# Kernel optimization log

Measured on AMD Instinct MI355X. Metric: run time of the kernel, lower is better.

Reference implementation:

```python
import jax, jax.numpy as jnp
import numpy as np

N = 10000
H_INPUTS = 128
H = 512
RW_LEN = 16
BATCH = 512


def setup_inputs() -> dict:
    key = jax.random.key(0)
    ks = jax.random.split(key, 5)
    x = jax.random.normal(ks[0], (BATCH, RW_LEN, N + 1), dtype=jnp.float32)
    # xavier-ish scaled params
    W_down = jax.random.normal(ks[1], (N, H_INPUTS), dtype=jnp.float32) * (1.0 / np.sqrt(N))
    W_cell = jax.random.normal(ks[2], (H_INPUTS + 1 + H, 4 * H), dtype=jnp.float32) * (1.0 / np.sqrt(H_INPUTS + 1 + H))
    b_cell = jnp.zeros((4 * H,), dtype=jnp.float32)
    W_out = jax.random.normal(ks[3], (H, 1), dtype=jnp.float32) * (1.0 / np.sqrt(H))
    b_out = jnp.zeros((1,), dtype=jnp.float32)
    return {"x": x, "W_down": W_down, "W_cell": W_cell, "b_cell": b_cell,
            "W_out": W_out, "b_out": b_out}


def _forward(x, W_down, W_cell, b_cell, W_out, b_out):
    B = x.shape[0]
    x_rw = x[:, :, :N]                       # [B, T, N]
    x_weights = x[:, :, -1:]                 # [B, T, 1]
    xa = jnp.einsum('btn,nh->bth', x_rw, W_down)  # down-projection [B, T, H_in]
    xc = jnp.concatenate([xa, x_weights], axis=2)  # [B, T, H_in+1]
    xc_t = jnp.swapaxes(xc, 0, 1)            # [T, B, H_in+1] for scan

    h0 = jnp.zeros((B, H), dtype=x.dtype)
    c0 = jnp.zeros((B, H), dtype=x.dtype)

    def step(carry, xt):
        h, c = carry
        gates = jnp.concatenate([xt, h], axis=1) @ W_cell + b_cell  # [B, 4H]
        i_g, c_g, f_g, o_g = jnp.split(gates, 4, axis=1)
        # custom forget-gate bias of +1
        c_new = c * jax.nn.sigmoid(f_g + 1.0) + jax.nn.sigmoid(i_g) * jnp.tanh(c_g)
        h_new = jax.nn.sigmoid(o_g) * jnp.tanh(c_new)
        return (h_new, c_new), None

    (h, _), _ = jax.lax.scan(step, (h0, c0), xc_t)
    pred = h @ W_out + b_out                 # [B, 1]
    return pred


def reference(x, W_down, W_cell, b_cell, W_out, b_out):
    return _forward(x, W_down, W_cell, b_cell, W_out, b_out)
```

## Files before the change

### kernel.cpp

```cpp
#include <hip/hip_runtime.h>
#include <cmath>

#define TID ((int)threadIdx.x)

typedef __bf16 bf16_t;
typedef bf16_t bf16x8 __attribute__((ext_vector_type(8)));
typedef float floatx4 __attribute__((ext_vector_type(4)));

#define MFMA(a, b, c) __builtin_amdgcn_mfma_f32_16x16x32_bf16(a, b, c, 0, 0, 0)

constexpr int N_IN = 10000;
constexpr int XP   = 10001;
constexpr int KPD  = 10240;
constexpr int HH   = 512;
constexpr int TT   = 16;
constexpr int NB   = 512;
constexpr int MROW = 8192;
constexpr int KSPLIT = 16;
constexpr int KCHUNK = 640;
constexpr int KT_A = 10;

__device__ __forceinline__ float sigm(float x) { return 1.0f / (1.0f + expf(-x)); }

__device__ __forceinline__ void gload16(const void* g, void* lds) {
  __builtin_amdgcn_global_load_lds(
      (const __attribute__((address_space(1))) unsigned int*)g,
      (__attribute__((address_space(3))) unsigned int*)lds, 16, 0, 0);
}

__global__ __launch_bounds__(256)
void kPrepWd(const float* __restrict__ Wd, bf16_t* __restrict__ Whi, bf16_t* __restrict__ Wlo) {
  __shared__ float Ts[64][133];
  const int k0 = blockIdx.x * 64;
  #pragma unroll
  for (int i = 0; i < 32; ++i) {
    int f = TID + 256 * i;
    int kk = f >> 7, c = f & 127;
    int k = k0 + kk;
    Ts[kk][c] = (k < N_IN) ? Wd[(size_t)k * 128 + c] : 0.0f;
  }
  __syncthreads();
  const int lane = TID & 63, w = TID >> 6;
  for (int pass = 0; pass < 32; ++pass) {
    int c = pass * 4 + w;
    float v = Ts[lane][c];
    bf16_t hi = (bf16_t)v;
    bf16_t lo = (bf16_t)(v - (float)hi);
    Whi[(size_t)c * KPD + k0 + lane] = hi;
    Wlo[(size_t)c * KPD + k0 + lane] = lo;
  }
}

__global__ __launch_bounds__(256)
void kPrepWc(const float* __restrict__ Wc, bf16_t* __restrict__ Wxh, bf16_t* __restrict__ Wxl,
             float* __restrict__ wN, bf16_t* __restrict__ Whh, bf16_t* __restrict__ Whl) {
  __shared__ float Ts[64][133];
  const int k0 = blockIdx.x * 64;
  const int c0 = blockIdx.y * 128;
  #pragma unroll
  for (int i = 0; i < 32; ++i) {
    int f = TID + 256 * i;
    int kk = f >> 7, cc = f & 127;
    int k = k0 + kk;
    Ts[kk][cc] = (k < 641) ? Wc[(size_t)k * 2048 + c0 + cc] : 0.0f;
  }
  __syncthreads();
  const int lane = TID & 63, w = TID >> 6;
  const int k = k0 + lane;
  for (int pass = 0; pass < 32; ++pass) {
    int cc = pass * 4 + w;
    int c = c0 + cc;
    float v = Ts[lane][cc];
    bf16_t hi = (bf16_t)v;
    bf16_t lo = (bf16_t)(v - (float)hi);
    if (k < 128) {
      Wxh[(size_t)c * 128 + k] = hi;
      Wxl[(size_t)c * 128 + k] = lo;
    } else if (k == 128) {
      wN[c] = v;
    } else if (k < 641) {
      Whh[(size_t)c * 512 + (k - 129)] = hi;
      Whl[(size_t)c * 512 + (k - 129)] = lo;
    }
  }
}

__global__ __launch_bounds__(256)
void kPrepXw(const float* __restrict__ x, float* __restrict__ xw) {
  int r = blockIdx.x * 256 + TID;
  xw[r] = x[(size_t)r * XP + N_IN];
}

__global__ __launch_bounds__(256, 2)
void kA_mfma(const float* __restrict__ x, const bf16_t* __restrict__ Whi,
             const bf16_t* __restrict__ Wlo, float* __restrict__ parts) {
  __shared__ __align__(16) bf16_t Bt[2][2048 * 8];
  const int lane = TID & 63, w = TID >> 6;
  const int row0 = blockIdx.x * 128 + w * 32;
  const int kbase = blockIdx.y * KCHUNK;
  floatx4 acc[2][8] = {};

  auto STAGE = [&](int buf, int kt) {
    const int k0 = kbase + kt * 64;
    #pragma unroll
    for (int i = 0; i < 8; ++i) {
      int L = i * 256 + TID;
      int arr = L >> 10, col = (L >> 3) & 127, g = L & 7;
      int gs = g ^ (col & 7);
      const bf16_t* src = (arr ? Wlo : Whi) + (size_t)col * KPD + k0 + gs * 8;
      gload16(src, &Bt[buf][(size_t)L * 8]);
    }
  };
  auto LOADX = [&](float4 (&xb)[2][2][2], int kt) {
    const int k0 = kbase + kt * 64;
    #pragma unroll
    for (int rf = 0; rf < 2; ++rf) {
      const float* xp = x + (size_t)(row0 + rf * 16 + (lane & 15)) * XP;
      #pragma unroll
      for (int h = 0; h < 2; ++h) {
        int kk0 = k0 + h * 32 + (lane >> 4) * 8;
        if (kk0 < N_IN) {
          xb[rf][h][0] = *(const float4*)(xp + kk0);
          xb[rf][h][1] = *(const float4*)(xp + kk0 + 4);
        } else {
          xb[rf][h][0] = make_float4(0.f, 0.f, 0.f, 0.f);
          xb[rf][h][1] = make_float4(0.f, 0.f, 0.f, 0.f);
        }
      }
    }
  };
  auto COMPUTE = [&](int buf, const float4 (&xb)[2][2][2]) {
    #pragma unroll
    for (int h = 0; h < 2; ++h) {
      const int p = h * 4 + (lane >> 4);
      bf16x8 ahi[2], alo[2];
      #pragma unroll
      for (int rf = 0; rf < 2; ++rf) {
        float vv[8] = {xb[rf][h][0].x, xb[rf][h][0].y, xb[rf][h][0].z, xb[rf][h][0].w,
                       xb[rf][h][1].x, xb[rf][h][1].y, xb[rf][h][1].z, xb[rf][h][1].w};
        #pragma unroll
        for (int e = 0; e < 8; ++e) {
          bf16_t hi = (bf16_t)vv[e];
          ahi[rf][e] = hi;
          alo[rf][e] = (bf16_t)(vv[e] - (float)hi);
        }
      }
      #pragma unroll
      for (int cf = 0; cf < 8; ++cf) {
        const int col = cf * 16 + (lane & 15);
        const int g = p ^ (col & 7);
        bf16x8 bhi = *(const bf16x8*)&Bt[buf][(col * 8 + g) * 8];
        bf16x8 blo = *(const bf16x8*)&Bt[buf][(1024 + col * 8 + g) * 8];
        #pragma unroll
        for (int rf = 0; rf < 2; ++rf) {
          acc[rf][cf] = MFMA(ahi[rf], bhi, acc[rf][cf]);
          acc[rf][cf] = MFMA(ahi[rf], blo, acc[rf][cf]);
          acc[rf][cf] = MFMA(alo[rf], bhi, acc[rf][cf]);
        }
      }
    }
  };

  float4 xbA[2][2][2], xbB[2][2][2];
  STAGE(0, 0);
  LOADX(xbA, 0);
  __syncthreads();
  #pragma unroll
  for (int kt = 0; kt < KT_A; kt += 2) {
    if (kt + 1 < KT_A) { STAGE(1, kt + 1); LOADX(xbB, kt + 1); }
    COMPUTE(0, xbA);
    __syncthreads();
    if (kt + 2 < KT_A) { STAGE(0, kt + 2); LOADX(xbA, kt + 2); }
    COMPUTE(1, xbB);
    __syncthreads();
  }

  float* dst = parts + (size_t)blockIdx.y * MROW * 128;
  #pragma unroll
  for (int rf = 0; rf < 2; ++rf)
    #pragma unroll
    for (int cf = 0; cf < 8; ++cf)
      #pragma unroll
      for (int r = 0; r < 4; ++r) {
        int row = row0 + rf * 16 + (lane >> 4) * 4 + r;
        int col = cf * 16 + (lane & 15);
        dst[(size_t)row * 128 + col] = acc[rf][cf][r];
      }
}

__global__ __launch_bounds__(256)
void kRed(const float* __restrict__ parts, float* __restrict__ xa) {
  size_t i4 = ((size_t)blockIdx.x * 256 + TID) * 4;
  float4 v = make_float4(0.f, 0.f, 0.f, 0.f);
  #pragma unroll
  for (int s = 0; s < KSPLIT; ++s) {
    float4 p = *(const float4*)&parts[(size_t)s * MROW * 128 + i4];
    v.x += p.x; v.y += p.y; v.z += p.z; v.w += p.w;
  }
  *(float4*)&xa[i4] = v;
}

__global__ __launch_bounds__(512, 2)
void kGx(const float* __restrict__ xa, const float* __restrict__ xw,
         const bf16_t* __restrict__ Wxh, const bf16_t* __restrict__ Wxl,
         const float* __restrict__ wN, const float* __restrict__ bc,
         float* __restrict__ gx) {
  __shared__ __align__(16) bf16_t Bt[4096 * 8];
  const int lane = TID & 63, w = TID >> 6;
  const int wr = w & 3, wc = w >> 2;
  const int rowbase = blockIdx.x * 128 + wr * 32;
  const int JB = blockIdx.y * 32;
  floatx4 acc[2][4] = {};

  #pragma unroll
  for (int i = 0; i < 8; ++i) {
    int L = i * 512 + TID;
    int arr = L >> 11, ce = (L >> 4) & 127, g = L & 15;
    int gs = g ^ (ce & 15);
    int c_src = (ce & 3) * 512 + JB + (ce >> 2);
    const bf16_t* src = (arr ? Wxl : Wxh) + (size_t)c_src * 128 + gs * 8;
    gload16(src, &Bt[(size_t)L * 8]);
  }
  float4 xb[2][2][2][2];
  #pragma unroll
  for (int kt = 0; kt < 2; ++kt)
    #pragma unroll
    for (int rf = 0; rf < 2; ++rf) {
      const float* ap = xa + (size_t)(rowbase + rf * 16 + (lane & 15)) * 128;
      #pragma unroll
      for (int h = 0; h < 2; ++h) {
        int kk0 = kt * 64 + h * 32 + (lane >> 4) * 8;
        xb[kt][rf][h][0] = *(const float4*)(ap + kk0);
        xb[kt][rf][h][1] = *(const float4*)(ap + kk0 + 4);
      }
    }
  __syncthreads();
  #pragma unroll
  for (int kt = 0; kt < 2; ++kt) {
    #pragma unroll
    for (int h = 0; h < 2; ++h) {
      const int p = kt * 8 + h * 4 + (lane >> 4);
      bf16x8 ahi[2], alo[2];
      #pragma unroll
      for (int rf = 0; rf < 2; ++rf) {
        float vv[8] = {xb[kt][rf][h][0].x, xb[kt][rf][h][0].y, xb[kt][rf][h][0].z, xb[kt][rf][h][0].w,
                       xb[kt][rf][h][1].x, xb[kt][rf][h][1].y, xb[kt][rf][h][1].z, xb[kt][rf][h][1].w};
        #pragma unroll
        for (int e = 0; e < 8; ++e) {
          bf16_t hi = (bf16_t)vv[e];
          ahi[rf][e] = hi;
          alo[rf][e] = (bf16_t)(vv[e] - (float)hi);
        }
      }
      #pragma unroll
      for (int cf = 0; cf < 4; ++cf) {
        const int ce = wc * 64 + cf * 16 + (lane & 15);
        const int g = p ^ (ce & 15);
        bf16x8 bhi = *(const bf16x8*)&Bt[(ce * 16 + g) * 8];
        bf16x8 blo = *(const bf16x8*)&Bt[(2048 + ce * 16 + g) * 8];
        #pragma unroll
        for (int rf = 0; rf < 2; ++rf) {
          acc[rf][cf] = MFMA(ahi[rf], bhi, acc[rf][cf]);
          acc[rf][cf] = MFMA(ahi[rf], blo, acc[rf][cf]);
          acc[rf][cf] = MFMA(alo[rf], bhi, acc[rf][cf]);
        }
      }
    }
  }
  #pragma unroll
  for (int rf = 0; rf < 2; ++rf)
    #pragma unroll
    for (int cf = 0; cf < 4; ++cf) {
      const int ce = wc * 64 + cf * 16 + (lane & 15);
      const int n = blockIdx.y * 128 + ce;
      const int c_src = (ce & 3) * 512 + JB + (ce >> 2);
      const float bias = bc[c_src];
      const float wn = wN[c_src];
      #pragma unroll
      for (int r = 0; r < 4; ++r) {
        int row = rowbase + rf * 16 + (lane >> 4) * 4 + r;
        gx[(size_t)row * 2048 + n] = acc[rf][cf][r] + bias + xw[row] * wn;
      }
    }
}

__global__ __launch_bounds__(128, 2)
void kStepH(const bf16_t* __restrict__ hhi_in, const bf16_t* __restrict__ hlo_in,
            const bf16_t* __restrict__ Whh, const bf16_t* __restrict__ Whl,
            const float* __restrict__ gx, const float* __restrict__ c_in,
            bf16_t* __restrict__ hhi_out, bf16_t* __restrict__ hlo_out,
            float* __restrict__ c_out, int t, int has_h) {
  __shared__ __align__(16) bf16_t Bt[2][1024 * 8];
  const int lane = TID & 63, w = TID >> 6;
  const int j0 = blockIdx.x * 16;
  const int brow0 = blockIdx.y * 64 + w * 32;
  floatx4 acc[2][4] = {};

  auto STAGE = [&](int buf, int kt) {
    const int k0 = kt * 64;
    #pragma unroll
    for (int i = 0; i < 8; ++i) {
      int L = i * 128 + TID;
      int arr = L >> 9, ce = (L >> 3) & 63, g = L & 7;
      int gs = g ^ (ce & 7);
      int c_src = (ce >> 4) * 512 + j0 + (ce & 15);
      const bf16_t* src = (arr ? Whl : Whh) + (size_t)c_src * 512 + k0 + gs * 8;
      gload16(src, &Bt[buf][(size_t)L * 8]);
    }
  };
  auto LOADA = [&](bf16x8 (&ar)[2][2][2], int kt) {
    #pragma unroll
    for (int rf = 0; rf < 2; ++rf) {
      const int b = brow0 + rf * 16 + (lane & 15);
      #pragma unroll
      for (int h = 0; h < 2; ++h) {
        const int kk0 = kt * 64 + h * 32 + (lane >> 4) * 8;
        ar[rf][h][0] = *(const bf16x8*)&hhi_in[(size_t)b * HH + kk0];
        ar[rf][h][1] = *(const bf16x8*)&hlo_in[(size_t)b * HH + kk0];
      }
    }
  };
  auto COMPUTE = [&](int buf, const bf16x8 (&ar)[2][2][2]) {
    #pragma unroll
    for (int h = 0; h < 2; ++h) {
      const int p = h * 4 + (lane >> 4);
      #pragma unroll
      for (int cf = 0; cf < 4; ++cf) {
        const int ce = cf * 16 + (lane & 15);
        const int g = p ^ (ce & 7);
        bf16x8 bhi = *(const bf16x8*)&Bt[buf][(ce * 8 + g) * 8];
        bf16x8 blo = *(const bf16x8*)&Bt[buf][(512 + ce * 8 + g) * 8];
        #pragma unroll
        for (int rf = 0; rf < 2; ++rf) {
          acc[rf][cf] = MFMA(ar[rf][h][0], bhi, acc[rf][cf]);
          acc[rf][cf] = MFMA(ar[rf][h][0], blo, acc[rf][cf]);
          acc[rf][cf] = MFMA(ar[rf][h][1], bhi, acc[rf][cf]);
        }
      }
    }
  };

  if (has_h) {
    bf16x8 aA[2][2][2], aB[2][2][2];
    STAGE(0, 0);
    LOADA(aA, 0);
    __syncthreads();
    #pragma unroll
    for (int kt = 0; kt < 8; kt += 2) {
      if (kt + 1 < 8) { STAGE(1, kt + 1); LOADA(aB, kt + 1); }
      COMPUTE(0, aA);
      __syncthreads();
      if (kt + 2 < 8) { STAGE(0, kt + 2); LOADA(aA, kt + 2); }
      COMPUTE(1, aB);
      __syncthreads();
    }
  }

  const int jl = lane & 15;
  const int j = j0 + jl;
  #pragma unroll
  for (int rf = 0; rf < 2; ++rf)
    #pragma unroll
    for (int r = 0; r < 4; ++r) {
      int b = brow0 + rf * 16 + (lane >> 4) * 4 + r;
      float4 gv = *(const float4*)&gx[((size_t)b * TT + t) * 2048 + (size_t)j * 4];
      float gi = acc[rf][0][r] + gv.x;
      float gc = acc[rf][1][r] + gv.y;
      float gf = acc[rf][2][r] + gv.z;
      float go = acc[rf][3][r] + gv.w;
      float cp = has_h ? c_in[(size_t)b * HH + j] : 0.0f;
      float cn = cp * sigm(gf + 1.0f) + sigm(gi) * tanhf(gc);
      float hn = sigm(go) * tanhf(cn);
      c_out[(size_t)b * HH + j] = cn;
      bf16_t hh = (bf16_t)hn;
      hhi_out[(size_t)b * HH + j] = hh;
      hlo_out[(size_t)b * HH + j] = (bf16_t)(hn - (float)hh);
    }
}

__global__ __launch_bounds__(64)
void kC_out(const bf16_t* __restrict__ hh, const bf16_t* __restrict__ hl,
            const float* __restrict__ Wo, const float* __restrict__ bo,
            float* __restrict__ out) {
  const int b = blockIdx.x;
  float s = 0.0f;
  for (int j = TID; j < HH; j += 64)
    s += ((float)hh[(size_t)b * HH + j] + (float)hl[(size_t)b * HH + j]) * Wo[j];
  #pragma unroll
  for (int off = 32; off > 0; off >>= 1) s += __shfl_down(s, off);
  if (TID == 0) out[b] = s + bo[0];
}

extern "C" void kernel_launch(void* const* d_in, const int* in_sizes, int n_in,
                              void* d_out, int out_size, void* d_ws, size_t ws_size,
                              hipStream_t stream) {
  const float* x  = (const float*)d_in[0];
  const float* Wd = (const float*)d_in[1];
  const float* Wc = (const float*)d_in[2];
  const float* bc = (const float*)d_in[3];
  const float* Wo = (const float*)d_in[4];
  const float* bo = (const float*)d_in[5];
  float* out = (float*)d_out;

  char* wsb = (char*)d_ws;
  size_t off = 0;
  auto alloc = [&](size_t bytes) -> void* {
    void* p = wsb + off;
    off = (off + bytes + 255) & ~(size_t)255;
    return p;
  };
  bf16_t* WdThi = (bf16_t*)alloc((size_t)128 * KPD * 2);
  bf16_t* WdTlo = (bf16_t*)alloc((size_t)128 * KPD * 2);
  bf16_t* WxThi = (bf16_t*)alloc((size_t)2048 * 128 * 2);
  bf16_t* WxTlo = (bf16_t*)alloc((size_t)2048 * 128 * 2);
  bf16_t* WhThi = (bf16_t*)alloc((size_t)2048 * 512 * 2);
  bf16_t* WhTlo = (bf16_t*)alloc((size_t)2048 * 512 * 2);
  float*  wN    = (float*)alloc(2048 * 4);
  float*  xw    = (float*)alloc(MROW * 4);
  float*  xa    = (float*)alloc((size_t)MROW * 128 * 4);
  float*  parts = (float*)alloc((size_t)KSPLIT * MROW * 128 * 4);
  float*  gx    = parts;
  bf16_t* hhi[2] = {(bf16_t*)alloc((size_t)NB * HH * 2), (bf16_t*)alloc((size_t)NB * HH * 2)};
  bf16_t* hlo[2] = {(bf16_t*)alloc((size_t)NB * HH * 2), (bf16_t*)alloc((size_t)NB * HH * 2)};
  float*  cb[2]  = {(float*)alloc((size_t)NB * HH * 4), (float*)alloc((size_t)NB * HH * 4)};

  kPrepWd<<<160, 256, 0, stream>>>(Wd, WdThi, WdTlo);
  kPrepWc<<<dim3(11, 16), 256, 0, stream>>>(Wc, WxThi, WxTlo, wN, WhThi, WhTlo);
  kPrepXw<<<32, 256, 0, stream>>>(x, xw);
  kA_mfma<<<dim3(64, KSPLIT), 256, 0, stream>>>(x, WdThi, WdTlo, parts);
  kRed<<<1024, 256, 0, stream>>>(parts, xa);
  kGx<<<dim3(64, 16), 512, 0, stream>>>(xa, xw, WxThi, WxTlo, wN, bc, gx);
  for (int t = 0; t < TT; ++t) {
    kStepH<<<dim3(32, 8), 128, 0, stream>>>(hhi[t & 1], hlo[t & 1], WhThi, WhTlo,
        gx, cb[t & 1], hhi[(t + 1) & 1], hlo[(t + 1) & 1], cb[(t + 1) & 1],
        t, (t == 0) ? 0 : 1);
  }
  kC_out<<<512, 64, 0, stream>>>(hhi[0], hlo[0], Wo, bo, out);
}
```

Measured before the change: 467.3 us.

## Fuse LSTM timesteps into persistent kernel with grid barrier and resident weights

Replaces the 16 per-step kStepH launches with one persistent kernel of 128 blocks. Each block loads its slice of the recurrent weights into shared memory once and keeps it there, and the blocks synchronise between steps through an atomic grid barrier. The gx layout becomes time-major so each step reads contiguous rows. The down-projection kernel also moves to 32-wide K tiles with a simpler unswizzled LDS layout. This removes per-step launch overhead and the repeated weight restaging, at the cost of depending on all 128 blocks being co-resident and of possible LDS bank conflicts in kA.

```diff
diff --git a/kernel.cpp b/kernel.cpp
--- a/kernel.cpp
+++ b/kernel.cpp
@@ -18,7 +18,8 @@
 constexpr int MROW = 8192;
 constexpr int KSPLIT = 16;
 constexpr int KCHUNK = 640;
-constexpr int KT_A = 10;
+constexpr int KT_A = 20;
+constexpr int NBLK_STEPS = 128;
 
 __device__ __forceinline__ float sigm(float x) { return 1.0f / (1.0f + expf(-x)); }
 
@@ -94,80 +95,72 @@
 __global__ __launch_bounds__(256, 2)
 void kA_mfma(const float* __restrict__ x, const bf16_t* __restrict__ Whi,
              const bf16_t* __restrict__ Wlo, float* __restrict__ parts) {
-  __shared__ __align__(16) bf16_t Bt[2][2048 * 8];
+  __shared__ __align__(16) bf16_t Bt[2 * 1024 * 8];
   const int lane = TID & 63, w = TID >> 6;
   const int row0 = blockIdx.x * 128 + w * 32;
   const int kbase = blockIdx.y * KCHUNK;
   floatx4 acc[2][8] = {};
 
   auto STAGE = [&](int buf, int kt) {
-    const int k0 = kbase + kt * 64;
-    #pragma unroll
-    for (int i = 0; i < 8; ++i) {
+    const int k0 = kbase + kt * 32;
+    #pragma unroll
+    for (int i = 0; i < 4; ++i) {
       int L = i * 256 + TID;
-      int arr = L >> 10, col = (L >> 3) & 127, g = L & 7;
-      int gs = g ^ (col & 7);
-      const bf16_t* src = (arr ? Wlo : Whi) + (size_t)col * KPD + k0 + gs * 8;
-      gload16(src, &Bt[buf][(size_t)L * 8]);
+      int arr = L >> 9, g = (L >> 7) & 3, col = L & 127;
+      const bf16_t* src = (arr ? Wlo : Whi) + (size_t)col * KPD + k0 + g * 8;
+      gload16(src, &Bt[((size_t)buf * 1024 + L) * 8]);
     }
   };
-  auto LOADX = [&](float4 (&xb)[2][2][2], int kt) {
-    const int k0 = kbase + kt * 64;
+  auto LOADX = [&](float4 (&xb)[2][2], int kt) {
+    const int kk0 = kbase + kt * 32 + (lane >> 4) * 8;
     #pragma unroll
     for (int rf = 0; rf < 2; ++rf) {
       const float* xp = x + (size_t)(row0 + rf * 16 + (lane & 15)) * XP;
-      #pragma unroll
-      for (int h = 0; h < 2; ++h) {
-        int kk0 = k0 + h * 32 + (lane >> 4) * 8;
-        if (kk0 < N_IN) {
-          xb[rf][h][0] = *(const float4*)(xp + kk0);
-          xb[rf][h][1] = *(const float4*)(xp + kk0 + 4);
-        } else {
-          xb[rf][h][0] = make_float4(0.f, 0.f, 0.f, 0.f);
-          xb[rf][h][1] = make_float4(0.f, 0.f, 0.f, 0.f);
-        }
+      if (kk0 < N_IN) {
+        xb[rf][0] = *(const float4*)(xp + kk0);
+        xb[rf][1] = *(const float4*)(xp + kk0 + 4);
+      } else {
+        xb[rf][0] = make_float4(0.f, 0.f, 0.f, 0.f);
+        xb[rf][1] = make_float4(0.f, 0.f, 0.f, 0.f);
       }
     }
   };
-  auto COMPUTE = [&](int buf, const float4 (&xb)[2][2][2]) {
-    #pragma unroll
-    for (int h = 0; h < 2; ++h) {
-      const int p = h * 4 + (lane >> 4);
-      bf16x8 ahi[2], alo[2];
+  auto COMPUTE = [&](int buf, const float4 (&xb)[2][2]) {
+    const int p = lane >> 4;
+    bf16x8 ahi[2], alo[2];
+    #pragma unroll
+    for (int rf = 0; rf < 2; ++rf) {
+      float vv[8] = {xb[rf][0].x, xb[rf][0].y, xb[rf][0].z, xb[rf][0].w,
+                     xb[rf][1].x, xb[rf][1].y, xb[rf][1].z, xb[rf][1].w};
+      #pragma unroll
+      for (int e = 0; e < 8; ++e) {
+        bf16_t hi = (bf16_t)vv[e];
+        ahi[rf][e] = hi;
+        alo[rf][e] = (bf16_t)(vv[e] - (float)hi);
+      }
+    }
+    #pragma unroll
+    for (int cf = 0; cf < 8; ++cf) {
+      const int col = cf * 16 + (lane & 15);
+      bf16x8 bhi = *(const bf16x8*)&Bt[((size_t)buf * 1024 + p * 128 + col) * 8];
+      bf16x8 blo = *(const bf16x8*)&Bt[((size_t)buf * 1024 + 512 + p * 128 + col) * 8];
       #pragma unroll
       for (int rf = 0; rf < 2; ++rf) {
-        float vv[8] = {xb[rf][h][0].x, xb[rf][h][0].y, xb[rf][h][0].z, xb[rf][h][0].w,
-                       xb[rf][h][1].x, xb[rf][h][1].y, xb[rf][h][1].z, xb[rf][h][1].w};
-        #pragma unroll
-        for (int e = 0; e < 8; ++e) {
-          bf16_t hi = (bf16_t)vv[e];
-          ahi[rf][e] = hi;
-          alo[rf][e] = (bf16_t)(vv[e] - (float)hi);
-        }
-      }
-      #pragma unroll
-      for (int cf = 0; cf < 8; ++cf) {
-        const int col = cf * 16 + (lane & 15);
-        const int g = p ^ (col & 7);
-        bf16x8 bhi = *(const bf16x8*)&Bt[buf][(col * 8 + g) * 8];
-        bf16x8 blo = *(const bf16x8*)&Bt[buf][(1024 + col * 8 + g) * 8];
-        #pragma unroll
-        for (int rf = 0; rf < 2; ++rf) {
-          acc[rf][cf] = MFMA(ahi[rf], bhi, acc[rf][cf]);
-          acc[rf][cf] = MFMA(ahi[rf], blo, acc[rf][cf]);
-          acc[rf][cf] = MFMA(alo[rf], bhi, acc[rf][cf]);
-        }
+        acc[rf][cf] = MFMA(ahi[rf], bhi, acc[rf][cf]);
+        acc[rf][cf] = MFMA(ahi[rf], blo, acc[rf][cf]);
+        acc[rf][cf] = MFMA(alo[rf], bhi, acc[rf][cf]);
       }
     }
   };
 
-  float4 xbA[2][2][2], xbB[2][2][2];
+  float4 xbA[2][2], xbB[2][2];
   STAGE(0, 0);
   LOADX(xbA, 0);
   __syncthreads();
   #pragma unroll
   for (int kt = 0; kt < KT_A; kt += 2) {
-    if (kt + 1 < KT_A) { STAGE(1, kt + 1); LOADX(xbB, kt + 1); }
+    STAGE(1, kt + 1);
+    LOADX(xbB, kt + 1);
     COMPUTE(0, xbA);
     __syncthreads();
     if (kt + 2 < KT_A) { STAGE(0, kt + 2); LOADX(xbA, kt + 2); }
@@ -279,103 +272,120 @@
       #pragma unroll
       for (int r = 0; r < 4; ++r) {
         int row = rowbase + rf * 16 + (lane >> 4) * 4 + r;
-        gx[(size_t)row * 2048 + n] = acc[rf][cf][r] + bias + xw[row] * wn;
-      }
-    }
-}
-
-__global__ __launch_bounds__(128, 2)
-void kStepH(const bf16_t* __restrict__ hhi_in, const bf16_t* __restrict__ hlo_in,
-            const bf16_t* __restrict__ Whh, const bf16_t* __restrict__ Whl,
-            const float* __restrict__ gx, const float* __restrict__ c_in,
-            bf16_t* __restrict__ hhi_out, bf16_t* __restrict__ hlo_out,
-            float* __restrict__ c_out, int t, int has_h) {
-  __shared__ __align__(16) bf16_t Bt[2][1024 * 8];
+        int b = row >> 4, tt = row & 15;
+        gx[((size_t)tt * NB + b) * 2048 + n] = acc[rf][cf][r] + bias + xw[row] * wn;
+      }
+    }
+}
+
+__global__ __launch_bounds__(256, 1)
+void kSteps(const bf16_t* __restrict__ Whh, const bf16_t* __restrict__ Whl,
+            const float* __restrict__ gx,
+            bf16_t* __restrict__ h0hi, bf16_t* __restrict__ h0lo,
+            bf16_t* __restrict__ h1hi, bf16_t* __restrict__ h1lo,
+            float* __restrict__ c0, float* __restrict__ c1,
+            unsigned* __restrict__ bar) {
+  __shared__ __align__(16) bf16_t Bt[8192 * 8];
   const int lane = TID & 63, w = TID >> 6;
   const int j0 = blockIdx.x * 16;
-  const int brow0 = blockIdx.y * 64 + w * 32;
-  floatx4 acc[2][4] = {};
-
-  auto STAGE = [&](int buf, int kt) {
-    const int k0 = kt * 64;
-    #pragma unroll
-    for (int i = 0; i < 8; ++i) {
-      int L = i * 128 + TID;
-      int arr = L >> 9, ce = (L >> 3) & 63, g = L & 7;
-      int gs = g ^ (ce & 7);
-      int c_src = (ce >> 4) * 512 + j0 + (ce & 15);
-      const bf16_t* src = (arr ? Whl : Whh) + (size_t)c_src * 512 + k0 + gs * 8;
-      gload16(src, &Bt[buf][(size_t)L * 8]);
-    }
-  };
-  auto LOADA = [&](bf16x8 (&ar)[2][2][2], int kt) {
-    #pragma unroll
-    for (int rf = 0; rf < 2; ++rf) {
-      const int b = brow0 + rf * 16 + (lane & 15);
-      #pragma unroll
-      for (int h = 0; h < 2; ++h) {
-        const int kk0 = kt * 64 + h * 32 + (lane >> 4) * 8;
-        ar[rf][h][0] = *(const bf16x8*)&hhi_in[(size_t)b * HH + kk0];
-        ar[rf][h][1] = *(const bf16x8*)&hlo_in[(size_t)b * HH + kk0];
-      }
-    }
-  };
-  auto COMPUTE = [&](int buf, const bf16x8 (&ar)[2][2][2]) {
-    #pragma unroll
-    for (int h = 0; h < 2; ++h) {
-      const int p = h * 4 + (lane >> 4);
-      #pragma unroll
-      for (int cf = 0; cf < 4; ++cf) {
-        const int ce = cf * 16 + (lane & 15);
-        const int g = p ^ (ce & 7);
-        bf16x8 bhi = *(const bf16x8*)&Bt[buf][(ce * 8 + g) * 8];
-        bf16x8 blo = *(const bf16x8*)&Bt[buf][(512 + ce * 8 + g) * 8];
+  const int brow0 = blockIdx.y * 128 + w * 32;
+
+  for (int i = 0; i < 32; ++i) {
+    int L = i * 256 + TID;
+    int kt = L >> 10, arr = (L >> 9) & 1, ce = (L >> 3) & 63, g = L & 7;
+    int gs = g ^ (ce & 7);
+    int c_src = (ce >> 4) * 512 + j0 + (ce & 15);
+    const bf16_t* src = (arr ? Whl : Whh) + (size_t)c_src * 512 + kt * 64 + gs * 8;
+    gload16(src, &Bt[(size_t)L * 8]);
+  }
+  __syncthreads();
+
+  bf16_t* hhi[2] = {h0hi, h1hi};
+  bf16_t* hlo[2] = {h0lo, h1lo};
+  float*  cb[2]  = {c0, c1};
+
+  #pragma unroll 1
+  for (int t = 0; t < TT; ++t) {
+    floatx4 acc[2][4] = {};
+    if (t > 0) {
+      __syncthreads();
+      if (TID == 0) {
+        __threadfence();
+        __hip_atomic_fetch_add(bar, 1u, __ATOMIC_ACQ_REL, __HIP_MEMORY_SCOPE_AGENT);
+        const unsigned target = (unsigned)t * NBLK_STEPS;
+        while (__hip_atomic_load(bar, __ATOMIC_ACQUIRE, __HIP_MEMORY_SCOPE_AGENT) < target) {
+          __builtin_amdgcn_s_sleep(8);
+        }
+        __threadfence();
+      }
+      __syncthreads();
+      const bf16_t* hi_in = hhi[t & 1];
+      const bf16_t* lo_in = hlo[t & 1];
+      auto LOADA = [&](bf16x8 (&ar)[2][2][2], int kt) {
         #pragma unroll
         for (int rf = 0; rf < 2; ++rf) {
-          acc[rf][cf] = MFMA(ar[rf][h][0], bhi, acc[rf][cf]);
-          acc[rf][cf] = MFMA(ar[rf][h][0], blo, acc[rf][cf]);
-          acc[rf][cf] = MFMA(ar[rf][h][1], bhi, acc[rf][cf]);
+          const int b = brow0 + rf * 16 + (lane & 15);
+          #pragma unroll
+          for (int h = 0; h < 2; ++h) {
+            const int kk0 = kt * 64 + h * 32 + (lane >> 4) * 8;
+            ar[rf][h][0] = *(const bf16x8*)&hi_in[(size_t)b * HH + kk0];
+            ar[rf][h][1] = *(const bf16x8*)&lo_in[(size_t)b * HH + kk0];
+          }
         }
-      }
-    }
-  };
-
-  if (has_h) {
-    bf16x8 aA[2][2][2], aB[2][2][2];
-    STAGE(0, 0);
-    LOADA(aA, 0);
-    __syncthreads();
-    #pragma unroll
-    for (int kt = 0; kt < 8; kt += 2) {
-      if (kt + 1 < 8) { STAGE(1, kt + 1); LOADA(aB, kt + 1); }
-      COMPUTE(0, aA);
-      __syncthreads();
-      if (kt + 2 < 8) { STAGE(0, kt + 2); LOADA(aA, kt + 2); }
-      COMPUTE(1, aB);
-      __syncthreads();
-    }
-  }
-
-  const int jl = lane & 15;
-  const int j = j0 + jl;
-  #pragma unroll
-  for (int rf = 0; rf < 2; ++rf)
-    #pragma unroll
-    for (int r = 0; r < 4; ++r) {
-      int b = brow0 + rf * 16 + (lane >> 4) * 4 + r;
-      float4 gv = *(const float4*)&gx[((size_t)b * TT + t) * 2048 + (size_t)j * 4];
-      float gi = acc[rf][0][r] + gv.x;
-      float gc = acc[rf][1][r] + gv.y;
-      float gf = acc[rf][2][r] + gv.z;
-      float go = acc[rf][3][r] + gv.w;
-      float cp = has_h ? c_in[(size_t)b * HH + j] : 0.0f;
-      float cn = cp * sigm(gf + 1.0f) + sigm(gi) * tanhf(gc);
-      float hn = sigm(go) * tanhf(cn);
-      c_out[(size_t)b * HH + j] = cn;
-      bf16_t hh = (bf16_t)hn;
-      hhi_out[(size_t)b * HH + j] = hh;
-      hlo_out[(size_t)b * HH + j] = (bf16_t)(hn - (float)hh);
-    }
+      };
+      auto COMPUTE = [&](int kt, const bf16x8 (&ar)[2][2][2]) {
+        #pragma unroll
+        for (int h = 0; h < 2; ++h) {
+          const int p = h * 4 + (lane >> 4);
+          #pragma unroll
+          for (int cf = 0; cf < 4; ++cf) {
+            const int ce = cf * 16 + (lane & 15);
+            const int g = p ^ (ce & 7);
+            bf16x8 bhi = *(const bf16x8*)&Bt[((size_t)kt * 1024 + ce * 8 + g) * 8];
+            bf16x8 blo = *(const bf16x8*)&Bt[((size_t)kt * 1024 + 512 + ce * 8 + g) * 8];
+            #pragma unroll
+            for (int rf = 0; rf < 2; ++rf) {
+              acc[rf][cf] = MFMA(ar[rf][h][0], bhi, acc[rf][cf]);
+              acc[rf][cf] = MFMA(ar[rf][h][0], blo, acc[rf][cf]);
+              acc[rf][cf] = MFMA(ar[rf][h][1], bhi, acc[rf][cf]);
+            }
+          }
+        }
+      };
+      bf16x8 aA[2][2][2], aB[2][2][2];
+      LOADA(aA, 0);
+      #pragma unroll
+      for (int kt = 0; kt < 8; kt += 2) {
+        LOADA(aB, kt + 1);
+        COMPUTE(kt, aA);
+        if (kt + 2 < 8) LOADA(aA, kt + 2);
+        COMPUTE(kt + 1, aB);
+      }
+    }
+    const int j = j0 + (lane & 15);
+    const float* cin = cb[t & 1];
+    float* cout = cb[(t + 1) & 1];
+    bf16_t* hho = hhi[(t + 1) & 1];
+    bf16_t* hlo_o = hlo[(t + 1) & 1];
+    #pragma unroll
+    for (int rf = 0; rf < 2; ++rf)
+      #pragma unroll
+      for (int r = 0; r < 4; ++r) {
+        int b = brow0 + rf * 16 + (lane >> 4) * 4 + r;
+        float4 gv = *(const float4*)&gx[((size_t)t * NB + b) * 2048 + (size_t)j * 4];
+        float gi = acc[rf][0][r] + gv.x;
+        float gc = acc[rf][1][r] + gv.y;
+        float gf = acc[rf][2][r] + gv.z;
+        float go = acc[rf][3][r] + gv.w;
+        float cp = (t > 0) ? cin[(size_t)b * HH + j] : 0.0f;
+        float cn = cp * sigm(gf + 1.0f) + sigm(gi) * tanhf(gc);
+        float hn = sigm(go) * tanhf(cn);
+        cout[(size_t)b * HH + j] = cn;
+        bf16_t hh = (bf16_t)hn;
+        hho[(size_t)b * HH + j] = hh;
+        hlo_o[(size_t)b * HH + j] = (bf16_t)(hn - (float)hh);
+      }
+  }
 }
 
 __global__ __launch_bounds__(64)
@@ -420,20 +430,22 @@
   float*  xa    = (float*)alloc((size_t)MROW * 128 * 4);
   float*  parts = (float*)alloc((size_t)KSPLIT * MROW * 128 * 4);
   float*  gx    = parts;
-  bf16_t* hhi[2] = {(bf16_t*)alloc((size_t)NB * HH * 2), (bf16_t*)alloc((size_t)NB * HH * 2)};
-  bf16_t* hlo[2] = {(bf16_t*)alloc((size_t)NB * HH * 2), (bf16_t*)alloc((size_t)NB * HH * 2)};
-  float*  cb[2]  = {(float*)alloc((size_t)NB * HH * 4), (float*)alloc((size_t)NB * HH * 4)};
-
+  bf16_t* h0hi = (bf16_t*)alloc((size_t)NB * HH * 2);
+  bf16_t* h0lo = (bf16_t*)alloc((size_t)NB * HH * 2);
+  bf16_t* h1hi = (bf16_t*)alloc((size_t)NB * HH * 2);
+  bf16_t* h1lo = (bf16_t*)alloc((size_t)NB * HH * 2);
+  float*  c0   = (float*)alloc((size_t)NB * HH * 4);
+  float*  c1   = (float*)alloc((size_t)NB * HH * 4);
+  unsigned* bar = (unsigned*)alloc(256);
+
+  hipMemsetAsync(bar, 0, 256, stream);
   kPrepWd<<<160, 256, 0, stream>>>(Wd, WdThi, WdTlo);
   kPrepWc<<<dim3(11, 16), 256, 0, stream>>>(Wc, WxThi, WxTlo, wN, WhThi, WhTlo);
   kPrepXw<<<32, 256, 0, stream>>>(x, xw);
   kA_mfma<<<dim3(64, KSPLIT), 256, 0, stream>>>(x, WdThi, WdTlo, parts);
   kRed<<<1024, 256, 0, stream>>>(parts, xa);
   kGx<<<dim3(64, 16), 512, 0, stream>>>(xa, xw, WxThi, WxTlo, wN, bc, gx);
-  for (int t = 0; t < TT; ++t) {
-    kStepH<<<dim3(32, 8), 128, 0, stream>>>(hhi[t & 1], hlo[t & 1], WhThi, WhTlo,
-        gx, cb[t & 1], hhi[(t + 1) & 1], hlo[(t + 1) & 1], cb[(t + 1) & 1],
-        t, (t == 0) ? 0 : 1);
-  }
-  kC_out<<<512, 64, 0, stream>>>(hhi[0], hlo[0], Wo, bo, out);
-}
+  kSteps<<<dim3(32, 4), 256, 0, stream>>>(WhThi, WhTlo, gx,
+      h0hi, h0lo, h1hi, h1lo, c0, c1, bar);
+  kC_out<<<512, 64, 0, stream>>>(h0hi, h0lo, Wo, bo, out);
+}
```

Result: slower. 653.4 us (+39.8%).

## Halve kA k-tile with linear LDS layout and make gx time-major

Applied to the files above, without the earlier changes.

The down-projection kernel now stages 32-wide k-tiles instead of 64, which halves the LDS footprint. It drops the XOR swizzle in favour of a plain group-major layout and runs twice as many pipeline iterations. The gate-input buffer gx is rewritten in [t][b][n] order so each recurrent step reads a contiguous slab. The goal is higher occupancy in kA and better locality in the step kernels, at the cost of more barriers and possible LDS bank conflicts without the swizzle.

```diff
diff --git a/kernel.cpp b/kernel.cpp
--- a/kernel.cpp
+++ b/kernel.cpp
@@ -18,7 +18,7 @@
 constexpr int MROW = 8192;
 constexpr int KSPLIT = 16;
 constexpr int KCHUNK = 640;
-constexpr int KT_A = 10;
+constexpr int KT_A = 20;
 
 __device__ __forceinline__ float sigm(float x) { return 1.0f / (1.0f + expf(-x)); }
 
@@ -94,80 +94,72 @@
 __global__ __launch_bounds__(256, 2)
 void kA_mfma(const float* __restrict__ x, const bf16_t* __restrict__ Whi,
              const bf16_t* __restrict__ Wlo, float* __restrict__ parts) {
-  __shared__ __align__(16) bf16_t Bt[2][2048 * 8];
+  __shared__ __align__(16) bf16_t Bt[2 * 1024 * 8];
   const int lane = TID & 63, w = TID >> 6;
   const int row0 = blockIdx.x * 128 + w * 32;
   const int kbase = blockIdx.y * KCHUNK;
   floatx4 acc[2][8] = {};
 
   auto STAGE = [&](int buf, int kt) {
-    const int k0 = kbase + kt * 64;
-    #pragma unroll
-    for (int i = 0; i < 8; ++i) {
+    const int k0 = kbase + kt * 32;
+    #pragma unroll
+    for (int i = 0; i < 4; ++i) {
       int L = i * 256 + TID;
-      int arr = L >> 10, col = (L >> 3) & 127, g = L & 7;
-      int gs = g ^ (col & 7);
-      const bf16_t* src = (arr ? Wlo : Whi) + (size_t)col * KPD + k0 + gs * 8;
-      gload16(src, &Bt[buf][(size_t)L * 8]);
-    }
-  };
-  auto LOADX = [&](float4 (&xb)[2][2][2], int kt) {
-    const int k0 = kbase + kt * 64;
+      int arr = L >> 9, g = (L >> 7) & 3, col = L & 127;
+      const bf16_t* src = (arr ? Wlo : Whi) + (size_t)col * KPD + k0 + g * 8;
+      gload16(src, &Bt[((size_t)buf * 1024 + L) * 8]);
+    }
+  };
+  auto LOADX = [&](float4 (&xb)[2][2], int kt) {
+    const int kk0 = kbase + kt * 32 + (lane >> 4) * 8;
     #pragma unroll
     for (int rf = 0; rf < 2; ++rf) {
       const float* xp = x + (size_t)(row0 + rf * 16 + (lane & 15)) * XP;
-      #pragma unroll
-      for (int h = 0; h < 2; ++h) {
-        int kk0 = k0 + h * 32 + (lane >> 4) * 8;
-        if (kk0 < N_IN) {
-          xb[rf][h][0] = *(const float4*)(xp + kk0);
-          xb[rf][h][1] = *(const float4*)(xp + kk0 + 4);
-        } else {
-          xb[rf][h][0] = make_float4(0.f, 0.f, 0.f, 0.f);
-          xb[rf][h][1] = make_float4(0.f, 0.f, 0.f, 0.f);
-        }
-      }
-    }
-  };
-  auto COMPUTE = [&](int buf, const float4 (&xb)[2][2][2]) {
-    #pragma unroll
-    for (int h = 0; h < 2; ++h) {
-      const int p = h * 4 + (lane >> 4);
-      bf16x8 ahi[2], alo[2];
+      if (kk0 < N_IN) {
+        xb[rf][0] = *(const float4*)(xp + kk0);
+        xb[rf][1] = *(const float4*)(xp + kk0 + 4);
+      } else {
+        xb[rf][0] = make_float4(0.f, 0.f, 0.f, 0.f);
+        xb[rf][1] = make_float4(0.f, 0.f, 0.f, 0.f);
+      }
+    }
+  };
+  auto COMPUTE = [&](int buf, const float4 (&xb)[2][2]) {
+    const int p = lane >> 4;
+    bf16x8 ahi[2], alo[2];
+    #pragma unroll
+    for (int rf = 0; rf < 2; ++rf) {
+      float vv[8] = {xb[rf][0].x, xb[rf][0].y, xb[rf][0].z, xb[rf][0].w,
+                     xb[rf][1].x, xb[rf][1].y, xb[rf][1].z, xb[rf][1].w};
+      #pragma unroll
+      for (int e = 0; e < 8; ++e) {
+        bf16_t hi = (bf16_t)vv[e];
+        ahi[rf][e] = hi;
+        alo[rf][e] = (bf16_t)(vv[e] - (float)hi);
+      }
+    }
+    #pragma unroll
+    for (int cf = 0; cf < 8; ++cf) {
+      const int col = cf * 16 + (lane & 15);
+      bf16x8 bhi = *(const bf16x8*)&Bt[((size_t)buf * 1024 + p * 128 + col) * 8];
+      bf16x8 blo = *(const bf16x8*)&Bt[((size_t)buf * 1024 + 512 + p * 128 + col) * 8];
       #pragma unroll
       for (int rf = 0; rf < 2; ++rf) {
-        float vv[8] = {xb[rf][h][0].x, xb[rf][h][0].y, xb[rf][h][0].z, xb[rf][h][0].w,
-                       xb[rf][h][1].x, xb[rf][h][1].y, xb[rf][h][1].z, xb[rf][h][1].w};
-        #pragma unroll
-        for (int e = 0; e < 8; ++e) {
-          bf16_t hi = (bf16_t)vv[e];
-          ahi[rf][e] = hi;
-          alo[rf][e] = (bf16_t)(vv[e] - (float)hi);
-        }
-      }
-      #pragma unroll
-      for (int cf = 0; cf < 8; ++cf) {
-        const int col = cf * 16 + (lane & 15);
-        const int g = p ^ (col & 7);
-        bf16x8 bhi = *(const bf16x8*)&Bt[buf][(col * 8 + g) * 8];
-        bf16x8 blo = *(const bf16x8*)&Bt[buf][(1024 + col * 8 + g) * 8];
-        #pragma unroll
-        for (int rf = 0; rf < 2; ++rf) {
-          acc[rf][cf] = MFMA(ahi[rf], bhi, acc[rf][cf]);
-          acc[rf][cf] = MFMA(ahi[rf], blo, acc[rf][cf]);
-          acc[rf][cf] = MFMA(alo[rf], bhi, acc[rf][cf]);
-        }
-      }
-    }
-  };
-
-  float4 xbA[2][2][2], xbB[2][2][2];
+        acc[rf][cf] = MFMA(ahi[rf], bhi, acc[rf][cf]);
+        acc[rf][cf] = MFMA(ahi[rf], blo, acc[rf][cf]);
+        acc[rf][cf] = MFMA(alo[rf], bhi, acc[rf][cf]);
+      }
+    }
+  };
+
+  float4 xbA[2][2], xbB[2][2];
   STAGE(0, 0);
   LOADX(xbA, 0);
   __syncthreads();
   #pragma unroll
   for (int kt = 0; kt < KT_A; kt += 2) {
-    if (kt + 1 < KT_A) { STAGE(1, kt + 1); LOADX(xbB, kt + 1); }
+    STAGE(1, kt + 1);
+    LOADX(xbB, kt + 1);
     COMPUTE(0, xbA);
     __syncthreads();
     if (kt + 2 < KT_A) { STAGE(0, kt + 2); LOADX(xbA, kt + 2); }
@@ -279,7 +271,8 @@
       #pragma unroll
       for (int r = 0; r < 4; ++r) {
         int row = rowbase + rf * 16 + (lane >> 4) * 4 + r;
-        gx[(size_t)row * 2048 + n] = acc[rf][cf][r] + bias + xw[row] * wn;
+        int b = row >> 4, tt = row & 15;
+        gx[((size_t)tt * NB + b) * 2048 + n] = acc[rf][cf][r] + bias + xw[row] * wn;
       }
     }
 }
@@ -356,14 +349,13 @@
     }
   }
 
-  const int jl = lane & 15;
-  const int j = j0 + jl;
+  const int j = j0 + (lane & 15);
   #pragma unroll
   for (int rf = 0; rf < 2; ++rf)
     #pragma unroll
     for (int r = 0; r < 4; ++r) {
       int b = brow0 + rf * 16 + (lane >> 4) * 4 + r;
-      float4 gv = *(const float4*)&gx[((size_t)b * TT + t) * 2048 + (size_t)j * 4];
+      float4 gv = *(const float4*)&gx[((size_t)t * NB + b) * 2048 + (size_t)j * 4];
       float gi = acc[rf][0][r] + gv.x;
       float gc = acc[rf][1][r] + gv.y;
       float gf = acc[rf][2][r] + gv.z;
@@ -420,9 +412,15 @@
   float*  xa    = (float*)alloc((size_t)MROW * 128 * 4);
   float*  parts = (float*)alloc((size_t)KSPLIT * MROW * 128 * 4);
   float*  gx    = parts;
-  bf16_t* hhi[2] = {(bf16_t*)alloc((size_t)NB * HH * 2), (bf16_t*)alloc((size_t)NB * HH * 2)};
-  bf16_t* hlo[2] = {(bf16_t*)alloc((size_t)NB * HH * 2), (bf16_t*)alloc((size_t)NB * HH * 2)};
-  float*  cb[2]  = {(float*)alloc((size_t)NB * HH * 4), (float*)alloc((size_t)NB * HH * 4)};
+  bf16_t* h0hi = (bf16_t*)alloc((size_t)NB * HH * 2);
+  bf16_t* h0lo = (bf16_t*)alloc((size_t)NB * HH * 2);
+  bf16_t* h1hi = (bf16_t*)alloc((size_t)NB * HH * 2);
+  bf16_t* h1lo = (bf16_t*)alloc((size_t)NB * HH * 2);
+  float*  c0   = (float*)alloc((size_t)NB * HH * 4);
+  float*  c1   = (float*)alloc((size_t)NB * HH * 4);
+  bf16_t* hhi[2] = {h0hi, h1hi};
+  bf16_t* hlo[2] = {h0lo, h1lo};
+  float*  cb[2]  = {c0, c1};
 
   kPrepWd<<<160, 256, 0, stream>>>(Wd, WdThi, WdTlo);
   kPrepWc<<<dim3(11, 16), 256, 0, stream>>>(Wc, WxThi, WxTlo, wN, WhThi, WhTlo);
@@ -435,5 +433,5 @@
         gx, cb[t & 1], hhi[(t + 1) & 1], hlo[(t + 1) & 1], cb[(t + 1) & 1],
         t, (t == 0) ? 0 : 1);
   }
-  kC_out<<<512, 64, 0, stream>>>(hhi[0], hlo[0], Wo, bo, out);
-}
+  kC_out<<<512, 64, 0, stream>>>(h0hi, h0lo, Wo, bo, out);
+}
```

New measurement: 503.9 us. 1.08x slower.
